# Kernel optimization log

Hardware: AMD Instinct MI355X
Metric: run time of the kernel (lower is better)

Reference implementation:

```python
import jax, jax.numpy as jnp
import numpy as np

N_USERS = 50000
N_ITEMS = 100000
N_ENT = 200000
N_REL_TOTAL = 32  # n_relations * 2
DIM = 64
N_INTENTS = 2
N_LAYERS = 1
B = 4096
E_KG = 2_000_000
E_UI_HALF = 1_000_000  # user->item interactions; symmetrized to 2M directed edges


def setup_inputs() -> dict:
    key = jax.random.key(0)
    ks = jax.random.split(key, 16)
    s = 0.05  # xavier-ish scale
    user_emb = jax.random.normal(ks[0], (N_USERS, DIM), jnp.float32) * s
    entity_emb = jax.random.normal(ks[1], (N_ENT, DIM), jnp.float32) * s
    relation_emb = jax.random.normal(ks[2], (N_REL_TOTAL, DIM), jnp.float32) * s
    intent_weights = jax.random.normal(ks[3], (N_INTENTS, N_REL_TOTAL), jnp.float32) * s
    router_w = jax.random.normal(ks[4], (N_INTENTS, DIM), jnp.float32) * s
    router_b = jnp.zeros((N_INTENTS,), jnp.float32)
    kg_w = jax.random.normal(ks[5], (N_LAYERS, DIM, DIM), jnp.float32) * (1.0 / np.sqrt(DIM))
    item2entity = jax.random.randint(ks[6], (N_ITEMS,), 0, N_ENT)
    kg_src = jax.random.randint(ks[7], (E_KG,), 0, N_ENT)
    kg_dst = jax.random.randint(ks[8], (E_KG,), 0, N_ENT)
    kg_rel = jax.random.randint(ks[9], (E_KG,), 0, N_REL_TOTAL)
    # UI bipartite graph, symmetrically normalized (D^-1/2 A D^-1/2), as in _build_ui_graph
    rng = np.random.default_rng(0)
    uu = rng.integers(0, N_USERS, E_UI_HALF)
    ii = rng.integers(0, N_ITEMS, E_UI_HALF) + N_USERS
    rows = np.concatenate([uu, ii])
    cols = np.concatenate([ii, uu])
    n_nodes = N_USERS + N_ITEMS
    deg = np.bincount(rows, minlength=n_nodes).astype(np.float32)
    dinv = np.where(deg > 0, deg ** -0.5, 0.0).astype(np.float32)
    ui_vals = jnp.asarray(dinv[rows] * dinv[cols])
    ui_row = jnp.asarray(rows.astype(np.int32))
    ui_col = jnpseq = jnp.asarray(cols.astype(np.int32))
    u = jax.random.randint(ks[10], (B,), 0, N_USERS)
    i = jax.random.randint(ks[11], (B,), 0, N_ITEMS)
    neg_i = jax.random.randint(ks[12], (B,), 0, N_ITEMS)
    return dict(u=u, i=i, neg_i=neg_i,
                user_emb=user_emb, entity_emb=entity_emb, relation_emb=relation_emb,
                intent_weights=intent_weights, router_w=router_w, router_b=router_b,
                kg_w=kg_w, ui_vals=ui_vals,
                item2entity=item2entity, kg_src=kg_src, kg_dst=kg_dst, kg_rel=kg_rel,
                ui_row=ui_row, ui_col=ui_col)


def _l2norm(x):
    return x / jnp.maximum(jnp.linalg.norm(x, axis=-1, keepdims=True), 1e-12)


def reference(u, i, neg_i, user_emb, entity_emb, relation_emb, intent_weights,
              router_w, router_b, kg_w, ui_vals, item2entity, kg_src, kg_dst,
              kg_rel, ui_row, ui_col):
    n_ent = entity_emb.shape[0]
    # ---- _propagate_kg (dropout in eval mode = identity) ----
    x = entity_emb
    gate = jax.nn.sigmoid(relation_emb[kg_rel])  # [E, D]
    deg = jax.ops.segment_sum(jnp.ones(kg_dst.shape[0], jnp.float32), kg_dst,
                              num_segments=n_ent)
    deg = jnp.maximum(deg, 1.0)[:, None]
    for l in range(kg_w.shape[0]):
        msg = (x[kg_src] @ kg_w[l].T) * gate           # gather + linear + gate
        agg = jax.ops.segment_sum(msg, kg_dst, num_segments=n_ent)
        x = _l2norm(jax.nn.elu(agg / deg + x))
    item_kg = x[item2entity]                            # [n_items, D]
    # ---- _propagate_ui: sparse normalized adj propagation ----
    all_emb = jnp.concatenate([user_emb, item_kg], 0)
    n_nodes = all_emb.shape[0]
    embs = [all_emb]
    for _ in range(N_LAYERS):
        all_emb = jax.ops.segment_sum(ui_vals[:, None] * all_emb[ui_col], ui_row,
                                      num_segments=n_nodes)
        embs.append(all_emb)
    final = jnp.mean(jnp.stack(embs, 1), 1)
    n_users = user_emb.shape[0]
    u_prop, i_prop = final[:n_users], final[n_users:]
    # ---- intent mixing ----
    intent_dist = jax.nn.softmax(u_prop @ router_w.T + router_b, axis=-1)
    intent_emb = jax.nn.softmax(intent_weights, axis=-1) @ relation_emb
    ue = u_prop + intent_dist @ intent_emb
    ie = i_prop + item_kg
    pos = jnp.sum(ue[u] * ie[i], 1)
    neg = jnp.sum(ue[u] * ie[neg_i], 1)
    return pos, neg
```

## Files before the change

kernel.cpp:

```cpp
#include <hip/hip_runtime.h>
#include <math.h>

#define N_USERS 50000
#define N_ITEMS 100000
#define N_ENT   200000
#define N_NODES (N_USERS + N_ITEMS)
#define N_REL   32
#define DIM     64

#define NB_KG  391
#define NB_UI  586
#define NB_TOT (NB_KG + NB_UI)
#define CAPD   4096

__device__ __forceinline__ unsigned short f2bf(float f) {
    unsigned u = __float_as_uint(f);
    u += 0x7FFFu + ((u >> 16) & 1u);
    return (unsigned short)(u >> 16);
}
__device__ __forceinline__ float bf_lo(unsigned v) { return __uint_as_float(v << 16); }
__device__ __forceinline__ float bf_hi(unsigned v) { return __uint_as_float(v & 0xFFFF0000u); }
__device__ __forceinline__ int getbit(const unsigned* m, int i) {
    return (m[i >> 5] >> (i & 31)) & 1;
}

__global__ __launch_bounds__(256) void ent_matmul(const float* __restrict__ x,
                                                  const float* __restrict__ w,
                                                  unsigned short* __restrict__ y16,
                                                  int n_ent) {
    __shared__ float xt[64][128];
    __shared__ float wt[64][64];
    int tid  = threadIdx.x;
    int base = blockIdx.x * 128;

    #pragma unroll
    for (int q = 0; q < 4; q++) {
        int idx = q * 256 + tid;
        int j = idx >> 4, k4 = idx & 15;
        int s0 = (k4 << 2) & 28;
        float4 v = ((const float4*)w)[idx];
        wt[4 * k4 + 0][j ^ s0] = v.x;
        wt[4 * k4 + 1][j ^ s0] = v.y;
        wt[4 * k4 + 2][j ^ s0] = v.z;
        wt[4 * k4 + 3][j ^ s0] = v.w;
    }
    #pragma unroll
    for (int q = 0; q < 8; q++) {
        int idx = q * 256 + tid;
        int r = idx >> 4, k4 = idx & 15;
        int gr = base + r;
        int s0 = (k4 << 2) & 28;
        if (gr < n_ent) {
            float4 v = ((const float4*)x)[(long)gr * 16 + k4];
            xt[4 * k4 + 0][r ^ s0] = v.x;
            xt[4 * k4 + 1][r ^ s0] = v.y;
            xt[4 * k4 + 2][r ^ s0] = v.z;
            xt[4 * k4 + 3][r ^ s0] = v.w;
        }
    }
    __syncthreads();

    int j0 = (tid & 7) * 8;
    int r0 = (tid >> 3) * 4;
    float acc[4][8];
    #pragma unroll
    for (int i = 0; i < 4; i++)
        #pragma unroll
        for (int j = 0; j < 8; j++) acc[i][j] = 0.f;

    #pragma unroll 4
    for (int k = 0; k < 64; k++) {
        int s = k & 28;
        float4 xa = *(const float4*)&xt[k][r0 ^ s];
        float4 wa = *(const float4*)&wt[k][j0 ^ s];
        float4 wb = *(const float4*)&wt[k][(j0 + 4) ^ s];
        float xr[4] = {xa.x, xa.y, xa.z, xa.w};
        float wr[8] = {wa.x, wa.y, wa.z, wa.w, wb.x, wb.y, wb.z, wb.w};
        #pragma unroll
        for (int i = 0; i < 4; i++)
            #pragma unroll
            for (int j = 0; j < 8; j++)
                acc[i][j] += xr[i] * wr[j];
    }

    #pragma unroll
    for (int i = 0; i < 4; i++) {
        int gr = base + r0 + i;
        if (gr < n_ent) {
            uint4 o;
            o.x = (unsigned)f2bf(acc[i][0]) | ((unsigned)f2bf(acc[i][1]) << 16);
            o.y = (unsigned)f2bf(acc[i][2]) | ((unsigned)f2bf(acc[i][3]) << 16);
            o.z = (unsigned)f2bf(acc[i][4]) | ((unsigned)f2bf(acc[i][5]) << 16);
            o.w = (unsigned)f2bf(acc[i][6]) | ((unsigned)f2bf(acc[i][7]) << 16);
            *(uint4*)&y16[(long)gr * 64 + j0] = o;
        }
    }
}

__global__ __launch_bounds__(256) void build_masks(const int* __restrict__ i2e,
                                                   const int* __restrict__ u,
                                                   const int* __restrict__ ipos,
                                                   const int* __restrict__ ineg,
                                                   unsigned* __restrict__ ent_mask,
                                                   unsigned* __restrict__ node_mask,
                                                   int* __restrict__ bcnt,
                                                   int B) {
    int t = blockIdx.x * 256 + threadIdx.x;
    int stride = gridDim.x * 256;
    for (int i = threadIdx.x; i < NB_TOT; i += 256) bcnt[i] = 0;
    for (int i = t; i < N_ITEMS; i += stride) {
        int e = i2e[i];
        atomicOr(&ent_mask[e >> 5], 1u << (e & 31));
    }
    for (int i = t; i < 3 * B; i += stride) {
        int r = (i < B) ? u[i]
              : (i < 2 * B) ? N_USERS + ipos[i - B]
                            : N_USERS + ineg[i - 2 * B];
        atomicOr(&node_mask[r >> 5], 1u << (r & 31));
    }
}

__global__ __launch_bounds__(256) void bucket_hist(const int* __restrict__ kg_dst,
                                                   const int* __restrict__ ui_row,
                                                   const unsigned* __restrict__ ent_mask,
                                                   const unsigned* __restrict__ node_mask,
                                                   const float* __restrict__ rel_emb,
                                                   float2* __restrict__ gateg,
                                                   int* __restrict__ bcnt,
                                                   int e_kg, int e_ui) {
    __shared__ int h[NB_TOT];
    for (int i = threadIdx.x; i < NB_TOT; i += 256) h[i] = 0;
    __syncthreads();
    if (blockIdx.x == 0) {
        for (int idx = threadIdx.x; idx < N_REL * 32; idx += 256) {
            int rel = idx >> 5, hl2 = idx & 31;
            float g0 = 1.0f / (1.0f + __expf(-rel_emb[rel * 64 + 2 * hl2]));
            float g1 = 1.0f / (1.0f + __expf(-rel_emb[rel * 64 + 2 * hl2 + 1]));
            gateg[idx] = make_float2(g0, g1);
        }
    }
    int n = e_kg + e_ui;
    int t = blockIdx.x * 256 + threadIdx.x;
    int stride = gridDim.x * 256;
    for (int e = t; e < n; e += stride) {
        int bk;
        if (e < e_kg) {
            int d = kg_dst[e];
            if (!getbit(ent_mask, d)) continue;
            bk = d >> 9;
        } else {
            int r = ui_row[e - e_kg];
            if (!getbit(node_mask, r)) continue;
            bk = NB_KG + (r >> 8);
        }
        atomicAdd(&h[bk], 1);
    }
    __syncthreads();
    for (int i = threadIdx.x; i < NB_TOT; i += 256)
        if (h[i]) atomicAdd(&bcnt[i], h[i]);
}

__global__ __launch_bounds__(256) void bucket_scan(const int* __restrict__ bcnt,
                                                   int* __restrict__ boff_kg,
                                                   int* __restrict__ boff_ui,
                                                   int* __restrict__ bcur) {
    __shared__ int sh[1024];
    int t = threadIdx.x;
    for (int seg = 0; seg < 2; seg++) {
        int NB = seg ? NB_UI : NB_KG;
        const int* src = bcnt + (seg ? NB_KG : 0);
        int idx[4] = { t, t + 256, t + 512, t + 768 };
        int v[4];
        #pragma unroll
        for (int q = 0; q < 4; q++) {
            v[q] = (idx[q] < NB) ? src[idx[q]] : 0;
            sh[idx[q]] = v[q];
        }
        __syncthreads();
        for (int o = 1; o < 1024; o <<= 1) {
            int a[4];
            #pragma unroll
            for (int q = 0; q < 4; q++) a[q] = (idx[q] >= o) ? sh[idx[q] - o] : 0;
            __syncthreads();
            #pragma unroll
            for (int q = 0; q < 4; q++) sh[idx[q]] += a[q];
            __syncthreads();
        }
        int* boff = seg ? boff_ui : boff_kg;
        int  base = seg ? NB_KG : 0;
        #pragma unroll
        for (int q = 0; q < 4; q++) {
            if (idx[q] < NB) {
                int ex = sh[idx[q]] - v[q];
                boff[idx[q]] = ex;
                bcur[base + idx[q]] = ex;
                if (idx[q] == NB - 1) boff[NB] = sh[idx[q]];
            }
        }
        __syncthreads();
    }
}

__global__ __launch_bounds__(512) void bucket_scatter(const int* __restrict__ kg_src,
                                                      const int* __restrict__ kg_dst,
                                                      const int* __restrict__ kg_rel,
                                                      const int* __restrict__ ui_row,
                                                      const int* __restrict__ ui_col,
                                                      const float* __restrict__ ui_vals,
                                                      const unsigned* __restrict__ ent_mask,
                                                      const unsigned* __restrict__ node_mask,
                                                      int* __restrict__ bcur,
                                                      unsigned int* __restrict__ kgrec,
                                                      int* __restrict__ uirec,
                                                      float* __restrict__ uval,
                                                      int e_kg, int e_ui) {
    __shared__ int h[NB_TOT];
    __shared__ int lbase[NB_TOT];
    int n = e_kg + e_ui;
    int nchunks = (n + 4095) >> 12;
    int tid = threadIdx.x;
    for (int c = blockIdx.x; c < nchunks; c += gridDim.x) {
        int base = c << 12;
        for (int i = tid; i < NB_TOT; i += 512) h[i] = 0;
        __syncthreads();
        unsigned int rec[8];
        float val[8];
        int bk[8];
        #pragma unroll
        for (int j = 0; j < 8; j++) {
            int e = base + j * 512 + tid;
            bk[j] = -1;
            if (e < n) {
                if (e < e_kg) {
                    int d = kg_dst[e];
                    if (getbit(ent_mask, d)) {
                        bk[j]  = d >> 9;
                        rec[j] = (unsigned int)kg_src[e] | ((unsigned int)kg_rel[e] << 18)
                                 | ((unsigned int)(d & 511) << 23);
                        atomicAdd(&h[bk[j]], 1);
                    }
                } else {
                    int i2 = e - e_kg;
                    int r  = ui_row[i2];
                    if (getbit(node_mask, r)) {
                        bk[j]  = NB_KG + (r >> 8);
                        rec[j] = (unsigned int)ui_col[i2] | ((unsigned int)(r & 255) << 18);
                        val[j] = ui_vals[i2];
                        atomicAdd(&h[bk[j]], 1);
                    }
                }
            }
        }
        __syncthreads();
        for (int i = tid; i < NB_TOT; i += 512) {
            int cc = h[i];
            lbase[i] = cc ? atomicAdd(&bcur[i], cc) : 0;
        }
        __syncthreads();
        #pragma unroll
        for (int j = 0; j < 8; j++) {
            if (bk[j] >= 0) {
                int pos = atomicAdd(&lbase[bk[j]], 1);
                if (bk[j] < NB_KG) kgrec[pos] = rec[j];
                else               { uirec[pos] = (int)rec[j]; uval[pos] = val[j]; }
            }
        }
        __syncthreads();
    }
}

__global__ __launch_bounds__(256) void bucket_finalize(const int* __restrict__ boff_kg,
                                                       const int* __restrict__ boff_ui,
                                                       unsigned int* __restrict__ kgrec,
                                                       int* __restrict__ uirec,
                                                       float* __restrict__ uval,
                                                       int* __restrict__ off_kg,
                                                       int* __restrict__ off_ui) {
    __shared__ unsigned int rec[CAPD];
    __shared__ float fval[CAPD];
    __shared__ int hist[512];
    bool iskg = blockIdx.x < NB_KG;
    int  b    = iskg ? blockIdx.x : blockIdx.x - NB_KG;
    const int* boff = iskg ? boff_kg : boff_ui;
    int ebeg = boff[b], eend = boff[b + 1];
    int ne   = min(eend - ebeg, CAPD);
    int key_base = iskg ? (b << 9) : (b << 8);
    int nkeys = iskg ? min(512, N_ENT - key_base) : min(256, N_NODES - key_base);
    int SH = iskg ? 23 : 18;
    int tid = threadIdx.x;

    for (int i = tid; i < ne; i += 256) {
        if (iskg) rec[i] = kgrec[ebeg + i];
        else { rec[i] = (unsigned int)uirec[ebeg + i]; fval[i] = uval[ebeg + i]; }
    }
    for (int i = tid; i < 512; i += 256) hist[i] = 0;
    __syncthreads();
    for (int i = tid; i < ne; i += 256)
        atomicAdd(&hist[rec[i] >> SH], 1);
    __syncthreads();
    int i0 = tid, i1 = tid + 256;
    int v0 = hist[i0], v1 = hist[i1];
    __syncthreads();
    for (int o = 1; o < 512; o <<= 1) {
        int a0 = (i0 >= o) ? hist[i0 - o] : 0;
        int a1 = (i1 >= o) ? hist[i1 - o] : 0;
        __syncthreads();
        hist[i0] += a0; hist[i1] += a1;
        __syncthreads();
    }
    int e0 = hist[i0] - v0, e1 = hist[i1] - v1;
    __syncthreads();
    hist[i0] = e0; hist[i1] = e1;
    int* offg = iskg ? off_kg : off_ui;
    if (i0 < nkeys) offg[key_base + i0] = ebeg + e0;
    if (i1 < nkeys) offg[key_base + i1] = ebeg + e1;
    if (blockIdx.x == 0 && tid == 0) {
        off_kg[N_ENT]   = boff_kg[NB_KG];
        off_ui[N_NODES] = boff_ui[NB_UI];
    }
    __syncthreads();
    for (int i = tid; i < ne; i += 256) {
        unsigned int r = rec[i];
        int k = r >> SH;
        int slot = atomicAdd(&hist[k], 1);
        if (iskg) kgrec[ebeg + slot] = r & 0x7FFFFFu;
        else      { uirec[ebeg + slot] = (int)(r & 0x3FFFFu); uval[ebeg + slot] = fval[i]; }
    }
}

__global__ __launch_bounds__(256) void kgagg_build(const int* __restrict__ off,
                                                   const unsigned int* __restrict__ packed,
                                                   const unsigned short* __restrict__ y16,
                                                   const float* __restrict__ entity_emb,
                                                   const float* __restrict__ user_emb,
                                                   const int* __restrict__ i2e,
                                                   const float4* __restrict__ gate4,
                                                   float* __restrict__ all_emb,
                                                   unsigned short* __restrict__ all16) {
    int lane = threadIdx.x & 63;
    int half = lane >> 5;
    int hl   = lane & 31;
    int duo  = hl >> 4;
    int ql   = hl & 15;
    long wpair = (long)((blockIdx.x * 256 + threadIdx.x) >> 6);
    int w = (int)(wpair * 2 + half);
    if (w >= N_NODES) return;

    if (w < N_USERS) {
        if (duo == 0) {
            float4 v = ((const float4*)user_emb)[(long)w * 16 + ql];
            ((uint2*)all16)[(long)w * 16 + ql] =
                make_uint2((unsigned)f2bf(v.x) | ((unsigned)f2bf(v.y) << 16),
                           (unsigned)f2bf(v.z) | ((unsigned)f2bf(v.w) << 16));
        }
        return;
    }

    int ent = i2e[w - N_USERS];
    const uint2* y2 = (const uint2*)y16;
    int beg = off[ent], end = off[ent + 1];
    float a0 = 0.f, a1 = 0.f, a2 = 0.f, a3 = 0.f;
    float b0 = 0.f, b1 = 0.f, b2 = 0.f, b3 = 0.f;
    int p = beg;
    for (; p + 4 <= end; p += 4) {
        unsigned pk0 = packed[p + duo];
        unsigned pk1 = packed[p + 2 + duo];
        uint2 v0 = y2[(long)(pk0 & 0x3FFFF) * 16 + ql];
        uint2 v1 = y2[(long)(pk1 & 0x3FFFF) * 16 + ql];
        float4 g0 = gate4[(pk0 >> 18) * 16 + ql];
        float4 g1 = gate4[(pk1 >> 18) * 16 + ql];
        a0 += bf_lo(v0.x) * g0.x;  a1 += bf_hi(v0.x) * g0.y;
        a2 += bf_lo(v0.y) * g0.z;  a3 += bf_hi(v0.y) * g0.w;
        b0 += bf_lo(v1.x) * g1.x;  b1 += bf_hi(v1.x) * g1.y;
        b2 += bf_lo(v1.y) * g1.z;  b3 += bf_hi(v1.y) * g1.w;
    }
    if (p + duo < end) {
        unsigned pk = packed[p + duo];
        uint2 v = y2[(long)(pk & 0x3FFFF) * 16 + ql];
        float4 g = gate4[(pk >> 18) * 16 + ql];
        a0 += bf_lo(v.x) * g.x;  a1 += bf_hi(v.x) * g.y;
        a2 += bf_lo(v.y) * g.z;  a3 += bf_hi(v.y) * g.w;
    }
    if (p + 2 + duo < end) {
        unsigned pk = packed[p + 2 + duo];
        uint2 v = y2[(long)(pk & 0x3FFFF) * 16 + ql];
        float4 g = gate4[(pk >> 18) * 16 + ql];
        b0 += bf_lo(v.x) * g.x;  b1 += bf_hi(v.x) * g.y;
        b2 += bf_lo(v.y) * g.z;  b3 += bf_hi(v.y) * g.w;
    }
    a0 += b0; a1 += b1; a2 += b2; a3 += b3;
    a0 += __shfl_xor(a0, 16);
    a1 += __shfl_xor(a1, 16);
    a2 += __shfl_xor(a2, 16);
    a3 += __shfl_xor(a3, 16);

    float deg = fmaxf((float)(end - beg), 1.0f);
    float4 xv = ((const float4*)entity_emb)[(long)ent * 16 + ql];
    float v0 = a0 / deg + xv.x;
    float v1 = a1 / deg + xv.y;
    float v2 = a2 / deg + xv.z;
    float v3 = a3 / deg + xv.w;
    v0 = (v0 > 0.0f) ? v0 : (__expf(v0) - 1.0f);
    v1 = (v1 > 0.0f) ? v1 : (__expf(v1) - 1.0f);
    v2 = (v2 > 0.0f) ? v2 : (__expf(v2) - 1.0f);
    v3 = (v3 > 0.0f) ? v3 : (__expf(v3) - 1.0f);
    float ss = v0 * v0 + v1 * v1 + v2 * v2 + v3 * v3;
    ss += __shfl_xor(ss, 1);
    ss += __shfl_xor(ss, 2);
    ss += __shfl_xor(ss, 4);
    ss += __shfl_xor(ss, 8);
    float inv = 1.0f / fmaxf(sqrtf(ss), 1e-12f);
    if (duo == 0) {
        float r0 = v0 * inv, r1 = v1 * inv, r2 = v2 * inv, r3 = v3 * inv;
        ((float4*)all_emb)[(long)w * 16 + ql] = make_float4(r0, r1, r2, r3);
        ((uint2*)all16)[(long)w * 16 + ql] =
            make_uint2((unsigned)f2bf(r0) | ((unsigned)f2bf(r1) << 16),
                       (unsigned)f2bf(r2) | ((unsigned)f2bf(r3) << 16));
    }
}

__global__ __launch_bounds__(256) void ui_aggregate_s(const int* __restrict__ off,
                                                      const int* __restrict__ colrec,
                                                      const float* __restrict__ uval,
                                                      const float* __restrict__ all_emb,
                                                      const float* __restrict__ user_emb,
                                                      const unsigned short* __restrict__ all16,
                                                      const int* __restrict__ u,
                                                      const int* __restrict__ ipos,
                                                      const int* __restrict__ ineg,
                                                      float* __restrict__ final_emb, int B) {
    const uint2* a2p = (const uint2*)all16;
    int lane = threadIdx.x & 63;
    int half = lane >> 5;
    int hl   = lane & 31;
    int duo  = hl >> 4;
    int ql   = hl & 15;
    long wpair = (long)((blockIdx.x * 256 + threadIdx.x) >> 6);
    int s = (int)(wpair * 2 + half);
    if (s >= 3 * B) return;
    int r;
    if (s < B)          r = u[s];
    else if (s < 2 * B) r = N_USERS + ipos[s - B];
    else                r = N_USERS + ineg[s - 2 * B];

    int beg = off[r], end = off[r + 1];
    float a0 = 0.f, a1 = 0.f, a2 = 0.f, a3 = 0.f;
    float b0 = 0.f, b1 = 0.f, b2 = 0.f, b3 = 0.f;
    int p = beg;
    for (; p + 4 <= end; p += 4) {
        int   c0 = colrec[p + duo];
        int   c1 = colrec[p + 2 + duo];
        float d0 = uval[p + duo];
        float d1 = uval[p + 2 + duo];
        uint2 v0 = a2p[(long)c0 * 16 + ql];
        uint2 v1 = a2p[(long)c1 * 16 + ql];
        a0 += d0 * bf_lo(v0.x);  a1 += d0 * bf_hi(v0.x);
        a2 += d0 * bf_lo(v0.y);  a3 += d0 * bf_hi(v0.y);
        b0 += d1 * bf_lo(v1.x);  b1 += d1 * bf_hi(v1.x);
        b2 += d1 * bf_lo(v1.y);  b3 += d1 * bf_hi(v1.y);
    }
    if (p + duo < end) {
        int   c = colrec[p + duo];
        float d = uval[p + duo];
        uint2 v = a2p[(long)c * 16 + ql];
        a0 += d * bf_lo(v.x);  a1 += d * bf_hi(v.x);
        a2 += d * bf_lo(v.y);  a3 += d * bf_hi(v.y);
    }
    if (p + 2 + duo < end) {
        int   c = colrec[p + 2 + duo];
        float d = uval[p + 2 + duo];
        uint2 v = a2p[(long)c * 16 + ql];
        b0 += d * bf_lo(v.x);  b1 += d * bf_hi(v.x);
        b2 += d * bf_lo(v.y);  b3 += d * bf_hi(v.y);
    }
    a0 += b0; a1 += b1; a2 += b2; a3 += b3;
    a0 += __shfl_xor(a0, 16);
    a1 += __shfl_xor(a1, 16);
    a2 += __shfl_xor(a2, 16);
    a3 += __shfl_xor(a3, 16);
    if (duo == 0) {
        float4 ae = (r < N_USERS)
            ? ((const float4*)user_emb)[(long)r * 16 + ql]
            : ((const float4*)all_emb)[(long)r * 16 + ql];
        ((float4*)final_emb)[(long)r * 16 + ql] =
            make_float4(0.5f * (ae.x + a0), 0.5f * (ae.y + a1),
                        0.5f * (ae.z + a2), 0.5f * (ae.w + a3));
    }
}

__global__ void final_kernel(const int* __restrict__ u, const int* __restrict__ ipos,
                             const int* __restrict__ ineg,
                             const float* __restrict__ final_emb,
                             const float* __restrict__ all_emb,
                             const float* __restrict__ rw, const float* __restrict__ rb,
                             const float* __restrict__ iw, const float* __restrict__ rel_emb,
                             float* __restrict__ out, int B) {
    __shared__ float sh_intent[128];
    if (threadIdx.x < 64) {
        int j = threadIdx.x;
        for (int k = 0; k < 2; k++) {
            float m = -1e30f;
            for (int r = 0; r < N_REL; r++) m = fmaxf(m, iw[k * N_REL + r]);
            float Z = 0.f, acc = 0.f;
            for (int r = 0; r < N_REL; r++) {
                float e = __expf(iw[k * N_REL + r] - m);
                Z += e;
                acc += e * rel_emb[r * 64 + j];
            }
            sh_intent[k * 64 + j] = acc / Z;
        }
    }
    __syncthreads();
    int lane = threadIdx.x & 63;
    int wave = (blockIdx.x * blockDim.x + threadIdx.x) >> 6;
    int nw   = (gridDim.x * blockDim.x) >> 6;
    for (int b = wave; b < B; b += nw) {
        int uu = u[b];
        float up = final_emb[(long)uu * 64 + lane];
        float l0 = up * rw[lane];
        float l1 = up * rw[64 + lane];
        #pragma unroll
        for (int o = 32; o; o >>= 1) {
            l0 += __shfl_xor(l0, o);
            l1 += __shfl_xor(l1, o);
        }
        l0 += rb[0]; l1 += rb[1];
        float m  = fmaxf(l0, l1);
        float e0 = __expf(l0 - m), e1 = __expf(l1 - m);
        float inv = 1.0f / (e0 + e1);
        float p0 = e0 * inv, p1 = e1 * inv;
        float ue = up + p0 * sh_intent[lane] + p1 * sh_intent[64 + lane];

        int it = ipos[b];
        long rr = (long)(N_USERS + it) * 64 + lane;
        float ie = final_emb[rr] + all_emb[rr];
        float dp = ue * ie;
        #pragma unroll
        for (int o = 32; o; o >>= 1) dp += __shfl_xor(dp, o);
        if (lane == 0) out[b] = dp;

        it = ineg[b];
        rr = (long)(N_USERS + it) * 64 + lane;
        ie = final_emb[rr] + all_emb[rr];
        dp = ue * ie;
        #pragma unroll
        for (int o = 32; o; o >>= 1) dp += __shfl_xor(dp, o);
        if (lane == 0) out[B + b] = dp;
    }
}

extern "C" void kernel_launch(void* const* d_in, const int* in_sizes, int n_in,
                              void* d_out, int out_size, void* d_ws, size_t ws_size,
                              hipStream_t stream) {
    const int*   u          = (const int*)  d_in[0];
    const int*   ipos       = (const int*)  d_in[1];
    const int*   ineg       = (const int*)  d_in[2];
    const float* user_emb   = (const float*)d_in[3];
    const float* entity_emb = (const float*)d_in[4];
    const float* rel_emb    = (const float*)d_in[5];
    const float* iw         = (const float*)d_in[6];
    const float* rw         = (const float*)d_in[7];
    const float* rb         = (const float*)d_in[8];
    const float* kgw        = (const float*)d_in[9];
    const float* ui_vals    = (const float*)d_in[10];
    const int*   i2e        = (const int*)  d_in[11];
    const int*   kg_src     = (const int*)  d_in[12];
    const int*   kg_dst     = (const int*)  d_in[13];
    const int*   kg_rel     = (const int*)  d_in[14];
    const int*   ui_row     = (const int*)  d_in[15];
    const int*   ui_col     = (const int*)  d_in[16];
    float*       out        = (float*)d_out;

    int B    = in_sizes[0];
    int e_kg = in_sizes[12];
    int e_ui = in_sizes[15];

    char* ws = (char*)d_ws;
    unsigned short* y16       = (unsigned short*)(ws + 0);
    float*          all_emb   = (float*)(ws + 25600000);
    unsigned short* all16     = (unsigned short*)(ws + 64000000);
    float*          final_emb = (float*)(ws + 83200000);
    unsigned int*   kgrec     = (unsigned int*)(ws + 121600000);
    int*            uirec     = (int*)(ws + 129600000);
    float*          uval      = (float*)(ws + 133600000);
    int*            off_kg    = (int*)(ws + 137600000);
    int*            off_ui    = (int*)(ws + 138400256);
    unsigned*       ent_mask  = (unsigned*)(ws + 139000512);
    unsigned*       node_mask = (unsigned*)(ws + 139025600);
    int*            bcnt      = (int*)(ws + 139600512);
    int*            boff_kg   = (int*)(ws + 139604480);
    int*            boff_ui   = (int*)(ws + 139606272);
    int*            bcur      = (int*)(ws + 139608704);
    float2*         gateg     = (float2*)(ws + 139612672);

    hipMemsetAsync(ent_mask, 0, 25088 + 18752, stream);
    build_masks    <<<512, 256, 0, stream>>>(i2e, u, ipos, ineg, ent_mask, node_mask,
                                             bcnt, B);
    bucket_hist    <<<1024, 256, 0, stream>>>(kg_dst, ui_row, ent_mask, node_mask,
                                              rel_emb, gateg, bcnt, e_kg, e_ui);
    bucket_scan    <<<1,   256, 0, stream>>>(bcnt, boff_kg, boff_ui, bcur);
    bucket_scatter <<<768, 512, 0, stream>>>(kg_src, kg_dst, kg_rel, ui_row, ui_col,
                                             ui_vals, ent_mask, node_mask,
                                             bcur, kgrec, uirec, uval, e_kg, e_ui);
    bucket_finalize<<<NB_TOT, 256, 0, stream>>>(boff_kg, boff_ui, kgrec, uirec, uval,
                                                off_kg, off_ui);

    ent_matmul <<<(N_ENT + 127) / 128, 256, 0, stream>>>(entity_emb, kgw, y16, N_ENT);
    {
        int nwaves = (N_NODES + 1) / 2;
        int nblk   = (nwaves * 64 + 255) / 256;
        kgagg_build<<<nblk, 256, 0, stream>>>(
            off_kg, kgrec, y16, entity_emb, user_emb, i2e, (const float4*)gateg,
            all_emb, all16);
    }
    {
        int nwaves = (3 * B + 1) / 2;
        int nblk   = (nwaves * 64 + 255) / 256;
        ui_aggregate_s<<<nblk, 256, 0, stream>>>(
            off_ui, uirec, uval, all_emb, user_emb, all16, u, ipos, ineg, final_emb, B);
    }
    final_kernel<<<256, 256, 0, stream>>>(u, ipos, ineg, final_emb, all_emb,
                                          rw, rb, iw, rel_emb, out, B);
}
```

Measured before the change: 330.5 us.

## Fuse entity matmul into bucket scatter kernel and skip unneeded fp32 stores

Merges the bucket_scatter and ent_matmul launches into one kernel, mm_scatter. The first NSCAT blocks do the scatter and the remaining blocks do the matmul, so the two independent tasks can run concurrently and one launch is saved. The matmul is retiled for 512 threads with 2 rows per thread. kgagg_build now writes the fp32 all_emb row only for nodes set in node_mask, which cuts write traffic. The risks are higher shared-memory use per block (48KB), lower matmul occupancy, and all_emb rows being left unset for nodes the later kernels are assumed not to read.

```diff
diff --git a/kernel.cpp b/kernel.cpp
--- a/kernel.cpp
+++ b/kernel.cpp
@@ -12,6 +12,7 @@
 #define NB_UI  586
 #define NB_TOT (NB_KG + NB_UI)
 #define CAPD   4096
+#define NSCAT  768
 
 __device__ __forceinline__ unsigned short f2bf(float f) {
     unsigned u = __float_as_uint(f);
@@ -24,18 +25,91 @@
     return (m[i >> 5] >> (i & 31)) & 1;
 }
 
-__global__ __launch_bounds__(256) void ent_matmul(const float* __restrict__ x,
+__global__ __launch_bounds__(512) void mm_scatter(const float* __restrict__ x,
                                                   const float* __restrict__ w,
                                                   unsigned short* __restrict__ y16,
-                                                  int n_ent) {
-    __shared__ float xt[64][128];
-    __shared__ float wt[64][64];
-    int tid  = threadIdx.x;
-    int base = blockIdx.x * 128;
+                                                  int n_ent,
+                                                  const int* __restrict__ kg_src,
+                                                  const int* __restrict__ kg_dst,
+                                                  const int* __restrict__ kg_rel,
+                                                  const int* __restrict__ ui_row,
+                                                  const int* __restrict__ ui_col,
+                                                  const float* __restrict__ ui_vals,
+                                                  const unsigned* __restrict__ ent_mask,
+                                                  const unsigned* __restrict__ node_mask,
+                                                  int* __restrict__ bcur,
+                                                  unsigned int* __restrict__ kgrec,
+                                                  int* __restrict__ uirec,
+                                                  float* __restrict__ uval,
+                                                  int e_kg, int e_ui) {
+    __shared__ __align__(16) char smem[49152];
+    int tid = threadIdx.x;
+
+    if (blockIdx.x < NSCAT) {
+        int* h     = (int*)smem;
+        int* lbase = h + NB_TOT;
+        int n = e_kg + e_ui;
+        int nchunks = (n + 4095) >> 12;
+        for (int c = blockIdx.x; c < nchunks; c += NSCAT) {
+            int base = c << 12;
+            for (int i = tid; i < NB_TOT; i += 512) h[i] = 0;
+            __syncthreads();
+            unsigned int rec[8];
+            float val[8];
+            int bk[8];
+            #pragma unroll
+            for (int j = 0; j < 8; j++) {
+                int e = base + j * 512 + tid;
+                bk[j] = -1;
+                if (e < n) {
+                    if (e < e_kg) {
+                        int d = kg_dst[e];
+                        if (getbit(ent_mask, d)) {
+                            bk[j]  = d >> 9;
+                            rec[j] = (unsigned int)kg_src[e]
+                                     | ((unsigned int)kg_rel[e] << 18)
+                                     | ((unsigned int)(d & 511) << 23);
+                            atomicAdd(&h[bk[j]], 1);
+                        }
+                    } else {
+                        int i2 = e - e_kg;
+                        int r  = ui_row[i2];
+                        if (getbit(node_mask, r)) {
+                            bk[j]  = NB_KG + (r >> 8);
+                            rec[j] = (unsigned int)ui_col[i2]
+                                     | ((unsigned int)(r & 255) << 18);
+                            val[j] = ui_vals[i2];
+                            atomicAdd(&h[bk[j]], 1);
+                        }
+                    }
+                }
+            }
+            __syncthreads();
+            for (int i = tid; i < NB_TOT; i += 512) {
+                int cc = h[i];
+                lbase[i] = cc ? atomicAdd(&bcur[i], cc) : 0;
+            }
+            __syncthreads();
+            #pragma unroll
+            for (int j = 0; j < 8; j++) {
+                if (bk[j] >= 0) {
+                    int pos = atomicAdd(&lbase[bk[j]], 1);
+                    if (bk[j] < NB_KG) kgrec[pos] = rec[j];
+                    else               { uirec[pos] = (int)rec[j]; uval[pos] = val[j]; }
+                }
+            }
+            __syncthreads();
+        }
+        return;
+    }
+
+    float (*xt)[128] = (float (*)[128])smem;
+    float (*wt)[64]  = (float (*)[64])(smem + 32768);
+    int base = (blockIdx.x - NSCAT) * 128;
 
     #pragma unroll
-    for (int q = 0; q < 4; q++) {
-        int idx = q * 256 + tid;
+    for (int q = 0; q < 2; q++) {
+        int idx = q * 512 + tid;
         int j = idx >> 4, k4 = idx & 15;
         int s0 = (k4 << 2) & 28;
         float4 v = ((const float4*)w)[idx];
@@ -45,8 +119,8 @@
         wt[4 * k4 + 3][j ^ s0] = v.w;
     }
     #pragma unroll
-    for (int q = 0; q < 8; q++) {
-        int idx = q * 256 + tid;
+    for (int q = 0; q < 4; q++) {
+        int idx = q * 512 + tid;
         int r = idx >> 4, k4 = idx & 15;
         int gr = base + r;
         int s0 = (k4 << 2) & 28;
@@ -61,30 +135,30 @@
     __syncthreads();
 
     int j0 = (tid & 7) * 8;
-    int r0 = (tid >> 3) * 4;
-    float acc[4][8];
+    int r0 = (tid >> 3) * 2;
+    float acc[2][8];
     #pragma unroll
-    for (int i = 0; i < 4; i++)
+    for (int i = 0; i < 2; i++)
         #pragma unroll
         for (int j = 0; j < 8; j++) acc[i][j] = 0.f;
 
     #pragma unroll 4
     for (int k = 0; k < 64; k++) {
         int s = k & 28;
-        float4 xa = *(const float4*)&xt[k][r0 ^ s];
+        float2 xa = *(const float2*)&xt[k][r0 ^ s];
         float4 wa = *(const float4*)&wt[k][j0 ^ s];
         float4 wb = *(const float4*)&wt[k][(j0 + 4) ^ s];
-        float xr[4] = {xa.x, xa.y, xa.z, xa.w};
+        float xr[2] = {xa.x, xa.y};
         float wr[8] = {wa.x, wa.y, wa.z, wa.w, wb.x, wb.y, wb.z, wb.w};
         #pragma unroll
-        for (int i = 0; i < 4; i++)
+        for (int i = 0; i < 2; i++)
             #pragma unroll
             for (int j = 0; j < 8; j++)
                 acc[i][j] += xr[i] * wr[j];
     }
 
     #pragma unroll
-    for (int i = 0; i < 4; i++) {
+    for (int i = 0; i < 2; i++) {
         int gr = base + r0 + i;
         if (gr < n_ent) {
             uint4 o;
@@ -195,74 +269,6 @@
                 boff[idx[q]] = ex;
                 bcur[base + idx[q]] = ex;
                 if (idx[q] == NB - 1) boff[NB] = sh[idx[q]];
-            }
-        }
-        __syncthreads();
-    }
-}
-
-__global__ __launch_bounds__(512) void bucket_scatter(const int* __restrict__ kg_src,
-                                                      const int* __restrict__ kg_dst,
-                                                      const int* __restrict__ kg_rel,
-                                                      const int* __restrict__ ui_row,
-                                                      const int* __restrict__ ui_col,
-                                                      const float* __restrict__ ui_vals,
-                                                      const unsigned* __restrict__ ent_mask,
-                                                      const unsigned* __restrict__ node_mask,
-                                                      int* __restrict__ bcur,
-                                                      unsigned int* __restrict__ kgrec,
-                                                      int* __restrict__ uirec,
-                                                      float* __restrict__ uval,
-                                                      int e_kg, int e_ui) {
-    __shared__ int h[NB_TOT];
-    __shared__ int lbase[NB_TOT];
-    int n = e_kg + e_ui;
-    int nchunks = (n + 4095) >> 12;
-    int tid = threadIdx.x;
-    for (int c = blockIdx.x; c < nchunks; c += gridDim.x) {
-        int base = c << 12;
-        for (int i = tid; i < NB_TOT; i += 512) h[i] = 0;
-        __syncthreads();
-        unsigned int rec[8];
-        float val[8];
-        int bk[8];
-        #pragma unroll
-        for (int j = 0; j < 8; j++) {
-            int e = base + j * 512 + tid;
-            bk[j] = -1;
-            if (e < n) {
-                if (e < e_kg) {
-                    int d = kg_dst[e];
-                    if (getbit(ent_mask, d)) {
-                        bk[j]  = d >> 9;
-                        rec[j] = (unsigned int)kg_src[e] | ((unsigned int)kg_rel[e] << 18)
-                                 | ((unsigned int)(d & 511) << 23);
-                        atomicAdd(&h[bk[j]], 1);
-                    }
-                } else {
-                    int i2 = e - e_kg;
-                    int r  = ui_row[i2];
-                    if (getbit(node_mask, r)) {
-                        bk[j]  = NB_KG + (r >> 8);
-                        rec[j] = (unsigned int)ui_col[i2] | ((unsigned int)(r & 255) << 18);
-                        val[j] = ui_vals[i2];
-                        atomicAdd(&h[bk[j]], 1);
-                    }
-                }
-            }
-        }
-        __syncthreads();
-        for (int i = tid; i < NB_TOT; i += 512) {
-            int cc = h[i];
-            lbase[i] = cc ? atomicAdd(&bcur[i], cc) : 0;
-        }
-        __syncthreads();
-        #pragma unroll
-        for (int j = 0; j < 8; j++) {
-            if (bk[j] >= 0) {
-                int pos = atomicAdd(&lbase[bk[j]], 1);
-                if (bk[j] < NB_KG) kgrec[pos] = rec[j];
-                else               { uirec[pos] = (int)rec[j]; uval[pos] = val[j]; }
             }
         }
         __syncthreads();
@@ -335,6 +341,7 @@
                                                    const float* __restrict__ user_emb,
                                                    const int* __restrict__ i2e,
                                                    const float4* __restrict__ gate4,
+                                                   const unsigned* __restrict__ node_mask,
                                                    float* __restrict__ all_emb,
                                                    unsigned short* __restrict__ all16) {
     int lane = threadIdx.x & 63;
@@ -412,7 +419,8 @@
     float inv = 1.0f / fmaxf(sqrtf(ss), 1e-12f);
     if (duo == 0) {
         float r0 = v0 * inv, r1 = v1 * inv, r2 = v2 * inv, r3 = v3 * inv;
-        ((float4*)all_emb)[(long)w * 16 + ql] = make_float4(r0, r1, r2, r3);
+        if (getbit(node_mask, w))
+            ((float4*)all_emb)[(long)w * 16 + ql] = make_float4(r0, r1, r2, r3);
         ((uint2*)all16)[(long)w * 16 + ql] =
             make_uint2((unsigned)f2bf(r0) | ((unsigned)f2bf(r1) << 16),
                        (unsigned)f2bf(r2) | ((unsigned)f2bf(r3) << 16));
@@ -599,19 +607,19 @@
     bucket_hist    <<<1024, 256, 0, stream>>>(kg_dst, ui_row, ent_mask, node_mask,
                                               rel_emb, gateg, bcnt, e_kg, e_ui);
     bucket_scan    <<<1,   256, 0, stream>>>(bcnt, boff_kg, boff_ui, bcur);
-    bucket_scatter <<<768, 512, 0, stream>>>(kg_src, kg_dst, kg_rel, ui_row, ui_col,
-                                             ui_vals, ent_mask, node_mask,
-                                             bcur, kgrec, uirec, uval, e_kg, e_ui);
+    mm_scatter     <<<NSCAT + (N_ENT + 127) / 128, 512, 0, stream>>>(
+        entity_emb, kgw, y16, N_ENT,
+        kg_src, kg_dst, kg_rel, ui_row, ui_col, ui_vals,
+        ent_mask, node_mask, bcur, kgrec, uirec, uval, e_kg, e_ui);
     bucket_finalize<<<NB_TOT, 256, 0, stream>>>(boff_kg, boff_ui, kgrec, uirec, uval,
                                                 off_kg, off_ui);
 
-    ent_matmul <<<(N_ENT + 127) / 128, 256, 0, stream>>>(entity_emb, kgw, y16, N_ENT);
     {
         int nwaves = (N_NODES + 1) / 2;
         int nblk   = (nwaves * 64 + 255) / 256;
         kgagg_build<<<nblk, 256, 0, stream>>>(
             off_kg, kgrec, y16, entity_emb, user_emb, i2e, (const float4*)gateg,
-            all_emb, all16);
+            node_mask, all_emb, all16);
     }
     {
         int nwaves = (3 * B + 1) / 2;
```

Result: faster. 313.8 us (-5.1%).
